# Kernel tuning notes

Measured on AMD Instinct MI355X. Metric: run time of the kernel, lower is better.

## Reference

```python
import jax, jax.numpy as jnp
import numpy as np

NB, DM, DIN, DS, DTR, K = 4, 64, 128, 16, 4, 4
C, COUT, H, W, BATCH, NH = 256, 256, 32, 32, 4, 8


def layernorm(x, w, b, eps=1e-5):
    mu = x.mean(-1, keepdims=True)
    var = ((x - mu) ** 2).mean(-1, keepdims=True)
    return (x - mu) * jax.lax.rsqrt(var + eps) * w + b


def ln_hw(x, eps=1e-5):
    # F.layer_norm(x, [H, W]) -> normalize over last two dims, no affine
    mu = x.mean((-2, -1), keepdims=True)
    var = ((x - mu) ** 2).mean((-2, -1), keepdims=True)
    return (x - mu) * jax.lax.rsqrt(var + eps)


def conv1d(x, w, b, groups=1, pad=1):
    # x: (B, Cin, L), w: (Cout, Cin//groups, k)
    y = jax.lax.conv_general_dilated(x, w, (1,), [(pad, pad)],
                                     dimension_numbers=('NCH', 'OIH', 'NCH'),
                                     feature_group_count=groups)
    return y + b[None, :, None]


def selective_scan(u, dt, Bm, Cm, A, Dp):
    # u, dt: (B,L,din); Bm, Cm: (B,L,ds); A: (din,ds); Dp: (din,)
    dA = jnp.exp(dt[..., None] * A)                     # (B,L,din,ds)
    dBu = (dt * u)[..., None] * Bm[:, :, None, :]       # (B,L,din,ds)

    def step(h, inp):
        dA_t, dBu_t, C_t = inp
        h = dA_t * h + dBu_t
        return h, jnp.einsum('bds,bs->bd', h, C_t)

    h0 = jnp.zeros((u.shape[0], DIN, DS), u.dtype)
    _, ys = jax.lax.scan(step, h0, (dA.transpose(1, 0, 2, 3), dBu.transpose(1, 0, 2, 3), Cm.transpose(1, 0, 2)))
    return ys.transpose(1, 0, 2) + u * Dp


def mamba(xs, inw, convw, convb, xpw, dtw, dtb, alog, dp, outw):
    # xs: (B,L,DM) one branch of Mamba(d_model=DM, d_state=DS, d_conv=K, expand=2)
    xz = xs @ inw.T                                     # (B,L,2*DIN)
    u, z = jnp.split(xz, 2, axis=-1)
    # causal depthwise conv1d (torch pads K-1 and truncates to L == left pad K-1)
    uc = jax.lax.conv_general_dilated(u.transpose(0, 2, 1), convw[:, None, :], (1,), [(K - 1, 0)],
                                      dimension_numbers=('NCH', 'OIH', 'NCH'),
                                      feature_group_count=DIN) + convb[None, :, None]
    u = jax.nn.silu(uc.transpose(0, 2, 1))              # (B,L,DIN)
    xdbc = u @ xpw.T                                    # (B,L,DTR+2*DS)
    dt = jax.nn.softplus(xdbc[..., :DTR] @ dtw.T + dtb)
    Bm, Cm = xdbc[..., DTR:DTR + DS], xdbc[..., DTR + DS:]
    y = selective_scan(u, dt, Bm, Cm, -jnp.exp(alog), dp)
    return (y * jax.nn.silu(z)) @ outw.T


mamba_v = jax.vmap(mamba)  # over branch axis 0 of inputs and all params


def mha(x, inw, inb, outw, outb):
    B, N, Cc = x.shape
    hd = Cc // NH
    qkv = x @ inw.T + inb
    q, k, v = jnp.split(qkv, 3, axis=-1)
    q = q.reshape(B, N, NH, hd).transpose(0, 2, 1, 3)
    k = k.reshape(B, N, NH, hd).transpose(0, 2, 1, 3)
    v = v.reshape(B, N, NH, hd).transpose(0, 2, 1, 3)
    att = jax.nn.softmax((q @ k.transpose(0, 1, 3, 2)) * (1.0 / (hd ** 0.5)), axis=-1)
    o = (att @ v).transpose(0, 2, 1, 3).reshape(B, N, Cc)
    return o @ outw.T + outb


def reference(x, norm_w, norm_b, skip_scale, m_inw, m_convw, m_convb, m_xpw, m_dtw, m_dtb, m_alog, m_d, m_outw, qdw_w, qdw_b, qpw_w, qpw_b, rdw_w, rdw_b, rpw_w, rpw_b, fdw_w, fdw_b, fpw_w, fpw_b, lc_w, lc_b, attn_inw, attn_inb, attn_outw, attn_outb, lgn_w, lgn_b, fc_w, fc_b, dwc_w, dwc_b, proj_w, proj_b):
    B, Cc, Hh, Ww = x.shape
    N = Hh * Ww
    xs = x.reshape(B, Cc, N).transpose(0, 2, 1)         # (B,N,C)
    xn = layernorm(xs, norm_w, norm_b)
    # channel-chunk into NB branches: (NB,B,N,DM)
    xc = xn.reshape(B, N, NB, DM).transpose(2, 0, 1, 3)
    xm = mamba_v(xc, m_inw, m_convw, m_convb, m_xpw, m_dtw, m_dtb, m_alog, m_d, m_outw) + skip_scale * xc
    x_concat = xm.transpose(1, 2, 0, 3).reshape(B, N, Cc)
    # branch gating: depthwise grouped conv (C->NB) then pointwise (NB->NB)
    Q = conv1d(conv1d(x_concat.transpose(0, 2, 1), qdw_w, qdw_b, groups=NB, pad=1), qpw_w, qpw_b, groups=1, pad=0)
    g = jax.nn.sigmoid(Q)                               # (B,NB,N)
    xg = (g.transpose(1, 0, 2)[..., None] * xm).transpose(1, 2, 0, 3).reshape(B, N, Cc)
    xgt = xg.transpose(0, 2, 1)                          # (B,C,N)
    R = conv1d(conv1d(xgt, rdw_w, rdw_b, groups=Cc, pad=1), rpw_w, rpw_b, groups=1, pad=0) + xgt
    cat = jnp.concatenate([xs, R.transpose(0, 2, 1)], axis=-1).transpose(0, 2, 1)  # (B,2C,N)
    xm2 = conv1d(conv1d(cat, fdw_w, fdw_b, groups=2 * Cc, pad=1), fpw_w, fpw_b, groups=1, pad=0) + cat[:, :Cc, :]
    xm2 = xm2.transpose(0, 2, 1)                         # (B,N,C)
    # local-global feature mixing
    x_local = conv1d(xm2.transpose(0, 2, 1), lc_w, lc_b, groups=Cc, pad=1).transpose(0, 2, 1)
    x_global = mha(xm2, attn_inw, attn_inb, attn_outw, attn_outb)
    x_out = jnp.concatenate([x_local, x_global], axis=-1) @ fc_w.T + fc_b
    x_out = jax.nn.gelu(layernorm(x_out, lgn_w, lgn_b), approximate=False)
    # DepthwiseConvolution: layer_norm over [H,W] (no affine) then depthwise conv2d
    xi = x_out.transpose(0, 2, 1).reshape(B, Cc, Hh, Ww)
    xi = ln_hw(xi)
    xi = jax.lax.conv_general_dilated(xi, dwc_w, (1, 1), [(1, 1), (1, 1)],
                                      dimension_numbers=('NCHW', 'OIHW', 'NCHW'),
                                      feature_group_count=Cc) + dwc_b[None, :, None, None]
    x_mixed = xi.reshape(B, Cc, N).transpose(0, 2, 1)
    x_mixed = layernorm(x_mixed, norm_w, norm_b)        # self.norm reused
    x_mixed = x_mixed @ proj_w.T + proj_b
    return x_mixed.transpose(0, 2, 1).reshape(B, COUT, Hh, Ww)


def setup_inputs() -> dict:
    key = jax.random.key(0)
    ks = iter(jax.random.split(key, 64))

    def rn(shape, s=0.02):
        return jax.random.normal(next(ks), shape, jnp.float32) * s

    return dict(
        x=jax.random.normal(next(ks), (BATCH, C, H, W), jnp.float32),
        norm_w=jnp.ones((C,), jnp.float32), norm_b=jnp.zeros((C,), jnp.float32),
        skip_scale=jnp.ones((1,), jnp.float32),
        m_inw=rn((NB, 2 * DIN, DM)), m_convw=rn((NB, DIN, K), 0.2), m_convb=jnp.zeros((NB, DIN), jnp.float32),
        m_xpw=rn((NB, DTR + 2 * DS, DIN)), m_dtw=rn((NB, DIN, DTR), 0.2), m_dtb=rn((NB, DIN), 0.5),
        m_alog=jnp.tile(jnp.log(jnp.arange(1, DS + 1, dtype=jnp.float32)), (NB, DIN, 1)),
        m_d=jnp.ones((NB, DIN), jnp.float32), m_outw=rn((NB, DM, DIN)),
        qdw_w=rn((NB, C // NB, 3), 0.1), qdw_b=jnp.zeros((NB,), jnp.float32),
        qpw_w=rn((NB, NB, 1), 0.3), qpw_b=jnp.zeros((NB,), jnp.float32),
        rdw_w=rn((C, 1, 3), 0.2), rdw_b=jnp.zeros((C,), jnp.float32),
        rpw_w=rn((C, C, 1)), rpw_b=jnp.zeros((C,), jnp.float32),
        fdw_w=rn((2 * C, 1, 3), 0.2), fdw_b=jnp.zeros((2 * C,), jnp.float32),
        fpw_w=rn((C, 2 * C, 1)), fpw_b=jnp.zeros((C,), jnp.float32),
        lc_w=rn((C, 1, 3), 0.2), lc_b=jnp.zeros((C,), jnp.float32),
        attn_inw=rn((3 * C, C)), attn_inb=jnp.zeros((3 * C,), jnp.float32),
        attn_outw=rn((C, C)), attn_outb=jnp.zeros((C,), jnp.float32),
        lgn_w=jnp.ones((C,), jnp.float32), lgn_b=jnp.zeros((C,), jnp.float32),
        fc_w=rn((C, 2 * C)), fc_b=jnp.zeros((C,), jnp.float32),
        dwc_w=rn((C, 1, 3, 3), 0.2), dwc_b=jnp.zeros((C,), jnp.float32),
        proj_w=rn((COUT, C)), proj_b=jnp.zeros((COUT,), jnp.float32),
    )
```

## Files before the change

kernel.cpp:

```cpp
#include <hip/hip_runtime.h>
#include <math.h>


namespace {
constexpr int NB_ = 4, DM_ = 64, DIN_ = 128, DS_ = 16, DTR_ = 4;
constexpr int C_ = 256, N_ = 1024, B_ = 4, HD_ = 32;
constexpr int NCH = 16, LCH = 64;
constexpr int NSTATE = 16 * 128 * 16;
}

typedef __attribute__((ext_vector_type(8))) short bf16x8;
typedef __attribute__((ext_vector_type(4))) float f32x4;
typedef __attribute__((ext_vector_type(8))) unsigned short ushort8v;
typedef __attribute__((ext_vector_type(4))) unsigned short ushort4v;

__device__ __forceinline__ unsigned short f2b(float f) {
  unsigned int u = __float_as_uint(f);
  unsigned int r = u + 0x7FFFu + ((u >> 16) & 1u);
  return (unsigned short)(r >> 16);
}
__device__ __forceinline__ float b2f(unsigned short u) {
  return __uint_as_float(((unsigned int)u) << 16);
}

__device__ __forceinline__ float2 blockReduce2(float a, float b, float* red) {
#pragma unroll
  for (int m = 1; m < 64; m <<= 1) {
    a += __shfl_xor(a, m, 64);
    b += __shfl_xor(b, m, 64);
  }
  int w = threadIdx.x >> 6;
  if ((threadIdx.x & 63) == 0) { red[2 * w] = a; red[2 * w + 1] = b; }
  __syncthreads();
  float ra = red[0] + red[2] + red[4] + red[6];
  float rb = red[1] + red[3] + red[5] + red[7];
  return make_float2(ra, rb);
}

__device__ __forceinline__ float siluf(float x) { return x / (1.f + expf(-x)); }
__device__ __forceinline__ float sigmf(float x) { return 1.f / (1.f + expf(-x)); }
__device__ __forceinline__ float softplusf(float x) {
  return fmaxf(x, 0.f) + log1pf(expf(-fabsf(x)));
}

__global__ __launch_bounds__(256) void k_ln_t2(const float* __restrict__ in,
                                               const float* __restrict__ w,
                                               const float* __restrict__ bias,
                                               unsigned short* __restrict__ out_ln) {
  __shared__ float tile[256][9];
  __shared__ float redp[32][8][2];
  __shared__ float stats[8][2];
  int bx = blockIdx.x;
  int b = bx >> 7, n0 = (bx & 127) * 8;
  int c = threadIdx.x;
  {
    const float* p = in + ((long)(b * C_ + c)) * N_ + n0;
#pragma unroll
    for (int j = 0; j < 8; ++j) tile[c][j] = p[j];
  }
  __syncthreads();
  {
    int n = c & 7, g = c >> 3;
    float a = 0.f, q = 0.f;
#pragma unroll
    for (int i = 0; i < 8; ++i) {
      float v = tile[g * 8 + i][n];
      a += v; q += v * v;
    }
    redp[g][n][0] = a; redp[g][n][1] = q;
  }
  __syncthreads();
  if (c < 8) {
    float a = 0.f, q = 0.f;
#pragma unroll
    for (int g2 = 0; g2 < 32; ++g2) { a += redp[g2][c][0]; q += redp[g2][c][1]; }
    float mu = a * (1.f / C_);
    float rs = rsqrtf(q * (1.f / C_) - mu * mu + 1e-5f);
    stats[c][0] = mu; stats[c][1] = rs;
  }
  __syncthreads();
  float wv = w[c], bv = bias[c];
#pragma unroll
  for (int j = 0; j < 8; ++j) {
    float v = tile[c][j];
    long o = ((long)(b * N_ + n0 + j)) * C_ + c;
    out_ln[o] = f2b((v - stats[j][0]) * stats[j][1] * wv + bv);
  }
}

__global__ __launch_bounds__(256) void k_inproj_conv(const unsigned short* __restrict__ xn,
                                                     const float* __restrict__ inw,
                                                     const float* __restrict__ cw,
                                                     const float* __restrict__ cb,
                                                     unsigned short* __restrict__ U,
                                                     unsigned short* __restrict__ Z) {
  __shared__ unsigned short xa[64][72];
  __shared__ unsigned short wb[64][72];
  __shared__ float ut[67][65];
  int r0 = blockIdx.x * 64;
  int nb = blockIdx.y >> 2, q = blockIdx.y & 3, c0 = q * 64;
  int t = threadIdx.x;
  int wv = t >> 6, lane = t & 63, g = lane >> 4, ql = lane & 15;
  const f32x4 zf = {0.f, 0.f, 0.f, 0.f};
  f32x4 acc[4] = {zf, zf, zf, zf};
  int rr = t >> 2, kq = (t & 3) * 16;
  {
    const unsigned short* xsrc = xn + (long)(r0 + rr) * C_ + nb * 64 + kq;
#pragma unroll
    for (int j = 0; j < 2; ++j)
      *(ushort8v*)&xa[rr][kq + 8 * j] = *(const ushort8v*)(xsrc + 8 * j);
    const float* wsrc = inw + ((long)nb * 256 + c0 + rr) * 64 + kq;
#pragma unroll
    for (int j = 0; j < 4; ++j) {
      float4 v = *(const float4*)(wsrc + 4 * j);
      ushort4v u = {f2b(v.x), f2b(v.y), f2b(v.z), f2b(v.w)};
      *(ushort4v*)&wb[rr][kq + 4 * j] = u;
    }
  }
  __syncthreads();
#pragma unroll
  for (int ks = 0; ks < 2; ++ks) {
    bf16x8 a = *(const bf16x8*)&xa[wv * 16 + ql][ks * 32 + g * 8];
#pragma unroll
    for (int ct = 0; ct < 4; ++ct) {
      bf16x8 b = *(const bf16x8*)&wb[ct * 16 + ql][ks * 32 + g * 8];
      acc[ct] = __builtin_amdgcn_mfma_f32_16x16x32_bf16(a, b, acc[ct], 0, 0, 0);
    }
  }
  if (q < 2) {
#pragma unroll
    for (int ct = 0; ct < 4; ++ct)
#pragma unroll
      for (int reg = 0; reg < 4; ++reg)
        ut[3 + wv * 16 + g * 4 + reg][ct * 16 + ql] = acc[ct][reg];
    if (t < 192) {
      int hr = t >> 6, lc = t & 63;
      float hv = 0.f;
      if ((r0 & 1023) != 0) {
        const unsigned short* xrow = xn + (long)(r0 - 3 + hr) * C_ + nb * 64;
        const float* wrow = inw + ((long)nb * 256 + c0 + lc) * 64;
#pragma unroll 8
        for (int k = 0; k < 64; ++k) hv += b2f(xrow[k]) * wrow[k];
      }
      ut[hr][lc] = hv;
    }
    __syncthreads();
#pragma unroll
    for (int ct = 0; ct < 4; ++ct) {
      int lc = ct * 16 + ql;
      int d = c0 + lc;
      const float* cwp = cw + (nb * DIN_ + d) * 4;
      float w0 = cwp[0], w1 = cwp[1], w2 = cwp[2], w3 = cwp[3];
      float bv = cb[nb * DIN_ + d];
#pragma unroll
      for (int reg = 0; reg < 4; ++reg) {
        int lr = wv * 16 + g * 4 + reg;
        float a = bv + w3 * ut[3 + lr][lc] + w2 * ut[2 + lr][lc] +
                  w1 * ut[1 + lr][lc] + w0 * ut[lr][lc];
        long row = (long)nb * 4096 + r0 + lr;
        U[row * DIN_ + d] = f2b(siluf(a));
      }
    }
  } else {
#pragma unroll
    for (int ct = 0; ct < 4; ++ct) {
      int col = c0 - 128 + ct * 16 + ql;
#pragma unroll
      for (int reg = 0; reg < 4; ++reg) {
        long row = (long)nb * 4096 + r0 + wv * 16 + g * 4 + reg;
        Z[row * DIN_ + col] = f2b(acc[ct][reg]);
      }
    }
  }
}

__global__ __launch_bounds__(256) void k_xdbc_scanA(const unsigned short* __restrict__ U,
                                                    const float* __restrict__ xpw,
                                                    const float* __restrict__ dtw,
                                                    const float* __restrict__ dtb,
                                                    const float* __restrict__ alog,
                                                    float* __restrict__ DT,
                                                    float* __restrict__ BMb,
                                                    float* __restrict__ CMb,
                                                    float* __restrict__ Aprod,
                                                    float* __restrict__ Hend) {
  __shared__ unsigned short u_sb[64][136];
  __shared__ unsigned short wb[48][72];
  __shared__ float xd_s[64][40];
  __shared__ float dtw_s[128][4];
  __shared__ float dtb_s[128];
  __shared__ float dt_s[64][132];
  __shared__ float bm_s[64][20];
  int t = threadIdx.x;
  long row0 = (long)blockIdx.x * 64;
  int nb = blockIdx.x >> 6;
  int nbb = blockIdx.x >> 4, chunk = blockIdx.x & 15;
  for (int i = t; i < 512; i += 256) dtw_s[i >> 2][i & 3] = dtw[nb * 512 + i];
  if (t < 128) dtb_s[t] = dtb[nb * DIN_ + t];
  int wv = t >> 6, lane = t & 63, g = lane >> 4, ql = lane & 15;
  const f32x4 zf = {0.f, 0.f, 0.f, 0.f};
  f32x4 acc[3] = {zf, zf, zf};
  int rr = t >> 2, kq = (t & 3) * 16;
  for (int k0 = 0; k0 < 128; k0 += 64) {
    __syncthreads();
    const unsigned short* xsrc = U + (row0 + rr) * DIN_ + k0 + kq;
#pragma unroll
    for (int j = 0; j < 2; ++j)
      *(ushort8v*)&u_sb[rr][k0 + kq + 8 * j] = *(const ushort8v*)(xsrc + 8 * j);
    if (rr < 48) {
      if (rr < 36) {
        const float* wsrc = xpw + (long)nb * 36 * 128 + rr * 128 + k0 + kq;
#pragma unroll
        for (int j = 0; j < 4; ++j) {
          float4 v = *(const float4*)(wsrc + 4 * j);
          ushort4v u = {f2b(v.x), f2b(v.y), f2b(v.z), f2b(v.w)};
          *(ushort4v*)&wb[rr][kq + 4 * j] = u;
        }
      } else {
        ushort4v z = {0, 0, 0, 0};
#pragma unroll
        for (int j = 0; j < 4; ++j) *(ushort4v*)&wb[rr][kq + 4 * j] = z;
      }
    }
    __syncthreads();
#pragma unroll
    for (int ks = 0; ks < 2; ++ks) {
      bf16x8 a = *(const bf16x8*)&u_sb[wv * 16 + ql][k0 + ks * 32 + g * 8];
#pragma unroll
      for (int ct = 0; ct < 3; ++ct) {
        bf16x8 b = *(const bf16x8*)&wb[ct * 16 + ql][ks * 32 + g * 8];
        acc[ct] = __builtin_amdgcn_mfma_f32_16x16x32_bf16(a, b, acc[ct], 0, 0, 0);
      }
    }
  }
#pragma unroll
  for (int ct = 0; ct < 3; ++ct) {
    int col = ct * 16 + ql;
    if (col < 36) {
#pragma unroll
      for (int reg = 0; reg < 4; ++reg)
        xd_s[wv * 16 + g * 4 + reg][col] = acc[ct][reg];
    }
  }
  __syncthreads();
  {
    int r = t >> 2, sq = (t & 3) * 4;
    float4 bm4 = make_float4(xd_s[r][4 + sq], xd_s[r][5 + sq],
                             xd_s[r][6 + sq], xd_s[r][7 + sq]);
    *(float4*)&BMb[(row0 + r) * DS_ + sq] = bm4;
    *(float4*)&bm_s[r][sq] = bm4;
    float4 cm4 = make_float4(xd_s[r][20 + sq], xd_s[r][21 + sq],
                             xd_s[r][22 + sq], xd_s[r][23 + sq]);
    *(float4*)&CMb[(row0 + r) * DS_ + sq] = cm4;
  }
  {
    int r = t >> 2, dg = t & 3;
    float x0 = xd_s[r][0], x1 = xd_s[r][1], x2 = xd_s[r][2], x3 = xd_s[r][3];
    float* dst = DT + (row0 + r) * DIN_ + dg * 32;
#pragma unroll
    for (int j = 0; j < 8; ++j) {
      float o[4];
#pragma unroll
      for (int e = 0; e < 4; ++e) {
        int d = dg * 32 + j * 4 + e;
        float a = dtb_s[d] + x0 * dtw_s[d][0] + x1 * dtw_s[d][1] +
                  x2 * dtw_s[d][2] + x3 * dtw_s[d][3];
        o[e] = softplusf(a);
      }
      float4 o4 = make_float4(o[0], o[1], o[2], o[3]);
      *(float4*)(dst + j * 4) = o4;
      *(float4*)&dt_s[r][dg * 32 + j * 4] = o4;
    }
  }
  __syncthreads();
  {
    int dl = t >> 2, sg = t & 3;
#pragma unroll
    for (int dh = 0; dh < 2; ++dh) {
      int d = dh * 64 + dl;
      float A[4];
#pragma unroll
      for (int i = 0; i < 4; ++i)
        A[i] = -expf(alog[(nb * DIN_ + d) * DS_ + sg * 4 + i]);
      float h[4] = {0.f, 0.f, 0.f, 0.f};
      float ap[4] = {1.f, 1.f, 1.f, 1.f};
      for (int tt = 0; tt < LCH; ++tt) {
        float dtv = dt_s[tt][d];
        float uv  = b2f(u_sb[tt][d]);
        float cc = dtv * uv;
        float4 bm4 = *(const float4*)&bm_s[tt][sg * 4];
        float bmv[4] = {bm4.x, bm4.y, bm4.z, bm4.w};
#pragma unroll
        for (int i = 0; i < 4; ++i) {
          float dA = __expf(dtv * A[i]);
          h[i] = dA * h[i] + cc * bmv[i];
          ap[i] *= dA;
        }
      }
      long st = (long)chunk * NSTATE + ((nbb << 7) + d) * 16 + sg * 4;
      *(float4*)&Aprod[st] = make_float4(ap[0], ap[1], ap[2], ap[3]);
      *(float4*)&Hend[st]  = make_float4(h[0], h[1], h[2], h[3]);
    }
  }
}

__global__ __launch_bounds__(256) void k_scanC(float* __restrict__ DT,
                                               const unsigned short* __restrict__ U,
                                               const float* __restrict__ BMb,
                                               const float* __restrict__ CMb,
                                               const float* __restrict__ alog,
                                               const float* __restrict__ Dp,
                                               const float* __restrict__ Aprod,
                                               const float* __restrict__ Hend) {
  __shared__ float dt_s[64][64];
  __shared__ float u_s[64][64];
  __shared__ float bm_s[64][16];
  __shared__ float cm_s[64][16];
  int bx = blockIdx.x;
  int chunk = bx >> 5, rem = bx & 31, nbb = rem >> 1, dh = rem & 1;
  int nb = nbb >> 2;
  int t = threadIdx.x;
  int dl = t >> 2, sg = t & 3;
  int d = dh * 64 + dl;
  long base = (long)nbb * N_ + chunk * LCH;
#pragma unroll
  for (int j = 0; j < 4; ++j) {
    int f = t + 256 * j;
    int tt = f >> 4, dq = (f & 15) * 4;
    long src = (base + tt) * DIN_ + dh * 64 + dq;
    *(float4*)&dt_s[tt][dq] = *(const float4*)&DT[src];
    ushort4v u4 = *(const ushort4v*)&U[src];
    u_s[tt][dq + 0] = b2f(u4[0]);
    u_s[tt][dq + 1] = b2f(u4[1]);
    u_s[tt][dq + 2] = b2f(u4[2]);
    u_s[tt][dq + 3] = b2f(u4[3]);
  }
  {
    int tt = t >> 2, sq = (t & 3) * 4;
    *(float4*)&bm_s[tt][sq] = *(const float4*)&BMb[(base + tt) * DS_ + sq];
    *(float4*)&cm_s[tt][sq] = *(const float4*)&CMb[(base + tt) * DS_ + sq];
  }
  float A[4];
#pragma unroll
  for (int i = 0; i < 4; ++i)
    A[i] = -expf(alog[(nb * DIN_ + d) * DS_ + sg * 4 + i]);
  float Dv = Dp[nb * DIN_ + d];
  float h[4] = {0.f, 0.f, 0.f, 0.f};
  {
    long state4 = ((nbb << 7) + d) * 16 + sg * 4;
    for (int c = 0; c < chunk; ++c) {
      float4 a4 = *(const float4*)&Aprod[(long)c * NSTATE + state4];
      float4 e4 = *(const float4*)&Hend[(long)c * NSTATE + state4];
      h[0] = e4.x + a4.x * h[0];
      h[1] = e4.y + a4.y * h[1];
      h[2] = e4.z + a4.z * h[2];
      h[3] = e4.w + a4.w * h[3];
    }
  }
  __syncthreads();
  for (int tt = 0; tt < LCH; ++tt) {
    float dtv = dt_s[tt][dl];
    float uv  = u_s[tt][dl];
    float cc = dtv * uv;
    float4 bm4 = *(const float4*)&bm_s[tt][sg * 4];
    float4 cm4 = *(const float4*)&cm_s[tt][sg * 4];
    float bmv[4] = {bm4.x, bm4.y, bm4.z, bm4.w};
    float cmv[4] = {cm4.x, cm4.y, cm4.z, cm4.w};
    float p = 0.f;
#pragma unroll
    for (int i = 0; i < 4; ++i) {
      float dA = __expf(dtv * A[i]);
      h[i] = dA * h[i] + cc * bmv[i];
      p += h[i] * cmv[i];
    }
    p += __shfl_xor(p, 1, 64);
    p += __shfl_xor(p, 2, 64);
    if (sg == 0) DT[(base + tt) * DIN_ + d] = p + Dv * uv;
  }
}

__global__ __launch_bounds__(256) void k_outproj_mfma(const float* __restrict__ Y,
                                                      const unsigned short* __restrict__ Zb,
                                                      const float* __restrict__ outw,
                                                      const unsigned short* __restrict__ xn,
                                                      const float* __restrict__ skip,
                                                      float* __restrict__ XMC) {
  __shared__ unsigned short xa[32][72];
  __shared__ unsigned short wb[64][72];
  int r0 = blockIdx.x * 32;
  int nb = blockIdx.y;
  int t = threadIdx.x;
  int w = t >> 6, lane = t & 63, g = lane >> 4, ql = lane & 15;
  int rg = w & 1, cp = w >> 1;
  const f32x4 zf = {0.f, 0.f, 0.f, 0.f};
  f32x4 acc[2] = {zf, zf};
  int ar = t >> 3, ak = (t & 7) * 8;
  int wr = t >> 2, wk = (t & 3) * 16;
  for (int k0 = 0; k0 < 128; k0 += 64) {
    __syncthreads();
    long row = (long)nb * 4096 + r0 + ar;
    const float* ysrc = Y + row * DIN_ + k0 + ak;
    const unsigned short* zsrc = Zb + row * DIN_ + k0 + ak;
#pragma unroll
    for (int j = 0; j < 2; ++j) {
      float4 yv = *(const float4*)(ysrc + 4 * j);
      ushort4v z4 = *(const ushort4v*)(zsrc + 4 * j);
      ushort4v u = {f2b(yv.x * siluf(b2f(z4[0]))), f2b(yv.y * siluf(b2f(z4[1]))),
                    f2b(yv.z * siluf(b2f(z4[2]))), f2b(yv.w * siluf(b2f(z4[3])))};
      *(ushort4v*)&xa[ar][ak + 4 * j] = u;
    }
    const float* wsrc = outw + ((long)nb * 64 + wr) * 128 + k0 + wk;
#pragma unroll
    for (int j = 0; j < 4; ++j) {
      float4 v = *(const float4*)(wsrc + 4 * j);
      ushort4v u = {f2b(v.x), f2b(v.y), f2b(v.z), f2b(v.w)};
      *(ushort4v*)&wb[wr][wk + 4 * j] = u;
    }
    __syncthreads();
#pragma unroll
    for (int ks = 0; ks < 2; ++ks) {
      bf16x8 a = *(const bf16x8*)&xa[rg * 16 + ql][ks * 32 + g * 8];
#pragma unroll
      for (int ct = 0; ct < 2; ++ct) {
        bf16x8 b = *(const bf16x8*)&wb[(cp * 2 + ct) * 16 + ql][ks * 32 + g * 8];
        acc[ct] = __builtin_amdgcn_mfma_f32_16x16x32_bf16(a, b, acc[ct], 0, 0, 0);
      }
    }
  }
  float sk = skip[0];
#pragma unroll
  for (int ct = 0; ct < 2; ++ct) {
    int col = (cp * 2 + ct) * 16 + ql;
#pragma unroll
    for (int reg = 0; reg < 4; ++reg) {
      int bn = r0 + rg * 16 + g * 4 + reg;
      long oc = (long)bn * C_ + nb * 64 + col;
      XMC[oc] = acc[ct][reg] + sk * b2f(xn[oc]);
    }
  }
}

__global__ __launch_bounds__(128) void k_gate(const float* __restrict__ XMC,
                                              const float* __restrict__ qdw_w,
                                              const float* __restrict__ qdw_b,
                                              const float* __restrict__ qpw_w,
                                              const float* __restrict__ qpw_b,
                                              float* __restrict__ G) {
  int t = threadIdx.x;
  int gid = (blockIdx.x * 128 + t) >> 4;
  int cq = t & 3, p = (t >> 2) & 3;
  int b = gid >> 10, n = gid & 1023;
  float a = 0.f;
#pragma unroll
  for (int k = 0; k < 3; ++k) {
    int nn = n + k - 1;
    if (nn < 0 || nn >= N_) continue;
    const float* xr = XMC + ((long)b * N_ + nn) * C_ + p * 64 + cq * 16;
    const float* wr = qdw_w + (p * 64 + cq * 16) * 3 + k;
    float xv[16];
    *(float4*)&xv[0]  = *(const float4*)(xr);
    *(float4*)&xv[4]  = *(const float4*)(xr + 4);
    *(float4*)&xv[8]  = *(const float4*)(xr + 8);
    *(float4*)&xv[12] = *(const float4*)(xr + 12);
#pragma unroll
    for (int i = 0; i < 16; ++i) a += xv[i] * wr[i * 3];
  }
  a += __shfl_xor(a, 1, 64);
  a += __shfl_xor(a, 2, 64);
  float q1 = a + qdw_b[p];
  int lane = t & 63;
  float q1g[4];
#pragma unroll
  for (int pp = 0; pp < 4; ++pp) q1g[pp] = __shfl(q1, (lane & ~12) | (pp << 2), 64);
  int o = p;
  float r = qpw_b[o];
#pragma unroll
  for (int pp = 0; pp < 4; ++pp) r += qpw_w[o * 4 + pp] * q1g[pp];
  if (cq == 0) G[((long)b * 4 + o) * N_ + n] = sigmf(r);
}

__global__ __launch_bounds__(256) void k_xg(const float* __restrict__ XMC,
                                            const float* __restrict__ G,
                                            float* __restrict__ XG) {
  __shared__ float tile[64][33];
  int bx = blockIdx.x;
  int b = bx >> 7, ct = (bx >> 5) & 3, nt = bx & 31;
  int c0 = ct * 64, n0 = nt * 32;
  int t = threadIdx.x;
  {
    int cc = t & 63, nq = t >> 6;
#pragma unroll
    for (int j = 0; j < 8; ++j) {
      int nn = nq * 8 + j;
      tile[cc][nn] = XMC[((long)(b * N_ + n0 + nn)) * C_ + c0 + cc];
    }
  }
  __syncthreads();
  {
    int nl = t & 31, cq = t >> 5;
    float g = G[((long)(b * 4 + ct)) * N_ + n0 + nl];
#pragma unroll
    for (int j = 0; j < 8; ++j) {
      int cl = cq * 8 + j;
      XG[((long)(b * C_ + c0 + cl)) * N_ + n0 + nl] = g * tile[cl][nl];
    }
  }
}

template <int KD>
__global__ __launch_bounds__(256) void k_gemm_cm_dw(const float* __restrict__ inA,
                                                    const float* __restrict__ inB,
                                                    const float* __restrict__ dww,
                                                    const float* __restrict__ dwb,
                                                    const float* __restrict__ w,
                                                    const float* __restrict__ bias,
                                                    const float* __restrict__ residCM,
                                                    const float* __restrict__ residXCM,
                                                    float* __restrict__ outCM,
                                                    unsigned short* __restrict__ outRMb) {
  __shared__ unsigned short xa[32][72];
  __shared__ unsigned short wb[64][72];
  int rb = blockIdx.x;
  int b = rb >> 5, n0 = (rb & 31) * 32;
  int c0 = blockIdx.y * 64;
  int t = threadIdx.x;
  int w8 = t >> 6, lane = t & 63, g = lane >> 4, ql = lane & 15;
  int rg = w8 & 1, cp = w8 >> 1;
  const f32x4 zf = {0.f, 0.f, 0.f, 0.f};
  f32x4 acc[2] = {zf, zf};
  int cr = t >> 2, nq = (t & 3) * 8;
  int wr = t >> 2, wk = (t & 3) * 16;
  for (int k0 = 0; k0 < KD; k0 += 64) {
    __syncthreads();
    {
      int k = k0 + cr;
      const float* src = (inB != nullptr && k >= 256)
                             ? inB + ((long)(b * 256 + k - 256)) * 1024
                             : inA + ((long)(b * 256 + k)) * 1024;
      float w0 = dww[k * 3], w1 = dww[k * 3 + 1], w2 = dww[k * 3 + 2], bv = dwb[k];
#pragma unroll
      for (int j = 0; j < 2; ++j) {
        int nb4 = n0 + nq + 4 * j;
        float4 v = *(const float4*)&src[nb4];
        float vm1 = (nb4 > 0) ? src[nb4 - 1] : 0.f;
        float vp4 = (nb4 + 4 < 1024) ? src[nb4 + 4] : 0.f;
        xa[nq + 4 * j + 0][cr] = f2b(bv + w0 * vm1 + w1 * v.x + w2 * v.y);
        xa[nq + 4 * j + 1][cr] = f2b(bv + w0 * v.x + w1 * v.y + w2 * v.z);
        xa[nq + 4 * j + 2][cr] = f2b(bv + w0 * v.y + w1 * v.z + w2 * v.w);
        xa[nq + 4 * j + 3][cr] = f2b(bv + w0 * v.z + w1 * v.w + w2 * vp4);
      }
    }
    const float* wsrc = w + (long)(c0 + wr) * KD + k0 + wk;
#pragma unroll
    for (int j = 0; j < 4; ++j) {
      float4 v = *(const float4*)(wsrc + 4 * j);
      ushort4v u = {f2b(v.x), f2b(v.y), f2b(v.z), f2b(v.w)};
      *(ushort4v*)&wb[wr][wk + 4 * j] = u;
    }
    __syncthreads();
#pragma unroll
    for (int ks = 0; ks < 2; ++ks) {
      bf16x8 a = *(const bf16x8*)&xa[rg * 16 + ql][ks * 32 + g * 8];
#pragma unroll
      for (int ct = 0; ct < 2; ++ct) {
        bf16x8 bfr = *(const bf16x8*)&wb[(cp * 2 + ct) * 16 + ql][ks * 32 + g * 8];
        acc[ct] = __builtin_amdgcn_mfma_f32_16x16x32_bf16(a, bfr, acc[ct], 0, 0, 0);
      }
    }
  }
#pragma unroll
  for (int ct = 0; ct < 2; ++ct) {
    int col = c0 + (cp * 2 + ct) * 16 + ql;
    float bv = bias[col];
    if (outCM) {
      long base = ((long)(b * 256 + col)) * 1024 + n0 + rg * 16 + g * 4;
      float4 r4 = *(const float4*)(residCM + base);
      float4 o = make_float4(acc[ct][0] + bv + r4.x, acc[ct][1] + bv + r4.y,
                             acc[ct][2] + bv + r4.z, acc[ct][3] + bv + r4.w);
      *(float4*)(outCM + base) = o;
    } else {
      int nbase = n0 + rg * 16 + g * 4;
      float4 r4 = *(const float4*)&residXCM[((long)(b * 256 + col)) * 1024 + nbase];
      float rv[4] = {r4.x, r4.y, r4.z, r4.w};
#pragma unroll
      for (int reg = 0; reg < 4; ++reg) {
        long row = (long)b * 1024 + nbase + reg;
        outRMb[row * 256 + col] = f2b(acc[ct][reg] + bv + rv[reg]);
      }
    }
  }
}

__global__ __launch_bounds__(256) void k_gemm_qkv(const unsigned short* __restrict__ in,
                                                  const float* __restrict__ w,
                                                  const float* __restrict__ bias,
                                                  unsigned short* __restrict__ out) {
  __shared__ unsigned short xa[64][72];
  __shared__ unsigned short wb[64][72];
  int r0 = blockIdx.x * 64;
  int c0 = blockIdx.y * 64;
  int t = threadIdx.x;
  int wv = t >> 6, lane = t & 63, g = lane >> 4, ql = lane & 15;
  const f32x4 zf = {0.f, 0.f, 0.f, 0.f};
  f32x4 acc[4] = {zf, zf, zf, zf};
  int rr = t >> 2, kq = (t & 3) * 16;
  for (int k0 = 0; k0 < 256; k0 += 64) {
    __syncthreads();
    const unsigned short* xsrc = in + (long)(r0 + rr) * 256 + k0 + kq;
#pragma unroll
    for (int j = 0; j < 2; ++j)
      *(ushort8v*)&xa[rr][kq + 8 * j] = *(const ushort8v*)(xsrc + 8 * j);
    const float* wsrc = w + (long)(c0 + rr) * 256 + k0 + kq;
#pragma unroll
    for (int j = 0; j < 4; ++j) {
      float4 v = *(const float4*)(wsrc + 4 * j);
      ushort4v u = {f2b(v.x), f2b(v.y), f2b(v.z), f2b(v.w)};
      *(ushort4v*)&wb[rr][kq + 4 * j] = u;
    }
    __syncthreads();
#pragma unroll
    for (int ks = 0; ks < 2; ++ks) {
      bf16x8 a = *(const bf16x8*)&xa[wv * 16 + ql][ks * 32 + g * 8];
#pragma unroll
      for (int ct = 0; ct < 4; ++ct) {
        bf16x8 b = *(const bf16x8*)&wb[ct * 16 + ql][ks * 32 + g * 8];
        acc[ct] = __builtin_amdgcn_mfma_f32_16x16x32_bf16(a, b, acc[ct], 0, 0, 0);
      }
    }
  }
#pragma unroll
  for (int ct = 0; ct < 4; ++ct) {
    int col = c0 + ct * 16 + ql;
    float bv = bias[col];
#pragma unroll
    for (int reg = 0; reg < 4; ++reg) {
      long row = r0 + wv * 16 + g * 4 + reg;
      out[row * 768 + col] = f2b(acc[ct][reg] + bv);
    }
  }
}

__global__ __launch_bounds__(256) void k_gemm_attnout(const unsigned short* __restrict__ inA,
                                                      const float* __restrict__ w,
                                                      const float* __restrict__ bias,
                                                      unsigned short* __restrict__ out) {
  __shared__ unsigned short xa[32][72];
  __shared__ unsigned short wb[64][72];
  int r0 = blockIdx.x * 32;
  int c0 = blockIdx.y * 64;
  int t = threadIdx.x;
  int w8 = t >> 6, lane = t & 63, g = lane >> 4, ql = lane & 15;
  int rg = w8 & 1, cp = w8 >> 1;
  const f32x4 zf = {0.f, 0.f, 0.f, 0.f};
  f32x4 acc[2] = {zf, zf};
  int ar = t >> 3, ak = (t & 7) * 8;
  int wr = t >> 2, wk = (t & 3) * 16;
  for (int k0 = 0; k0 < 256; k0 += 64) {
    __syncthreads();
    const unsigned short* xsrc = inA + (long)(r0 + ar) * 256 + k0 + ak;
    *(ushort8v*)&xa[ar][ak] = *(const ushort8v*)xsrc;
    const float* wsrc = w + (long)(c0 + wr) * 256 + k0 + wk;
#pragma unroll
    for (int j = 0; j < 4; ++j) {
      float4 v = *(const float4*)(wsrc + 4 * j);
      ushort4v u = {f2b(v.x), f2b(v.y), f2b(v.z), f2b(v.w)};
      *(ushort4v*)&wb[wr][wk + 4 * j] = u;
    }
    __syncthreads();
#pragma unroll
    for (int ks = 0; ks < 2; ++ks) {
      bf16x8 a = *(const bf16x8*)&xa[rg * 16 + ql][ks * 32 + g * 8];
#pragma unroll
      for (int ct = 0; ct < 2; ++ct) {
        bf16x8 b = *(const bf16x8*)&wb[(cp * 2 + ct) * 16 + ql][ks * 32 + g * 8];
        acc[ct] = __builtin_amdgcn_mfma_f32_16x16x32_bf16(a, b, acc[ct], 0, 0, 0);
      }
    }
  }
#pragma unroll
  for (int ct = 0; ct < 2; ++ct) {
    int col = c0 + (cp * 2 + ct) * 16 + ql;
    float bv = bias[col];
#pragma unroll
    for (int reg = 0; reg < 4; ++reg) {
      long row = r0 + rg * 16 + g * 4 + reg;
      out[row * 256 + col] = f2b(acc[ct][reg] + bv);
    }
  }
}

__global__ __launch_bounds__(256) void k_gemm_fc(const unsigned short* __restrict__ XM2,
                                                 const unsigned short* __restrict__ XGL,
                                                 const float* __restrict__ lcw,
                                                 const float* __restrict__ lcb,
                                                 const float* __restrict__ w,
                                                 const float* __restrict__ bias,
                                                 unsigned short* __restrict__ out) {
  __shared__ unsigned short xa[32][72];
  __shared__ unsigned short wb[64][72];
  int r0 = blockIdx.x * 32;
  int c0 = blockIdx.y * 64;
  int t = threadIdx.x;
  int w8 = t >> 6, lane = t & 63, g = lane >> 4, ql = lane & 15;
  int rg = w8 & 1, cp = w8 >> 1;
  const f32x4 zf = {0.f, 0.f, 0.f, 0.f};
  f32x4 acc[2] = {zf, zf};
  int ar = t >> 3, ak = (t & 7) * 8;
  int wr = t >> 2, wk = (t & 3) * 16;
  for (int k0 = 0; k0 < 512; k0 += 64) {
    __syncthreads();
    int kk = k0 + ak;
    long row = r0 + ar;
    if (kk < 256) {
      int n = (int)(row & 1023);
      const unsigned short* pc = XM2 + row * 256 + kk;
      bool hm = n > 0, hp = n < 1023;
#pragma unroll
      for (int j = 0; j < 2; ++j) {
        ushort4v v4 = *(const ushort4v*)(pc + 4 * j);
        ushort4v zm = {0, 0, 0, 0};
        ushort4v vm4 = hm ? *(const ushort4v*)(pc - 256 + 4 * j) : zm;
        ushort4v vp4 = hp ? *(const ushort4v*)(pc + 256 + 4 * j) : zm;
        int c = kk + 4 * j;
#pragma unroll
        for (int e = 0; e < 4; ++e) {
          float vv = b2f(v4[e]);
          float vmv = hm ? b2f(vm4[e]) : 0.f;
          float vpv = hp ? b2f(vp4[e]) : 0.f;
          xa[ar][ak + 4 * j + e] = f2b(lcb[c + e] + lcw[(c + e) * 3] * vmv +
                                       lcw[(c + e) * 3 + 1] * vv +
                                       lcw[(c + e) * 3 + 2] * vpv);
        }
      }
    } else {
      const unsigned short* xsrc = XGL + row * 256 + (kk - 256);
      *(ushort8v*)&xa[ar][ak] = *(const ushort8v*)xsrc;
    }
    const float* wsrc = w + (long)(c0 + wr) * 512 + k0 + wk;
#pragma unroll
    for (int j = 0; j < 4; ++j) {
      float4 v = *(const float4*)(wsrc + 4 * j);
      ushort4v u = {f2b(v.x), f2b(v.y), f2b(v.z), f2b(v.w)};
      *(ushort4v*)&wb[wr][wk + 4 * j] = u;
    }
    __syncthreads();
#pragma unroll
    for (int ks = 0; ks < 2; ++ks) {
      bf16x8 a = *(const bf16x8*)&xa[rg * 16 + ql][ks * 32 + g * 8];
#pragma unroll
      for (int ct = 0; ct < 2; ++ct) {
        bf16x8 b = *(const bf16x8*)&wb[(cp * 2 + ct) * 16 + ql][ks * 32 + g * 8];
        acc[ct] = __builtin_amdgcn_mfma_f32_16x16x32_bf16(a, b, acc[ct], 0, 0, 0);
      }
    }
  }
#pragma unroll
  for (int ct = 0; ct < 2; ++ct) {
    int col = c0 + (cp * 2 + ct) * 16 + ql;
    float bv = bias[col];
#pragma unroll
    for (int reg = 0; reg < 4; ++reg) {
      long row = r0 + rg * 16 + g * 4 + reg;
      out[row * 256 + col] = f2b(acc[ct][reg] + bv);
    }
  }
}

__global__ __launch_bounds__(256) void k_attn_mfma(const unsigned short* __restrict__ qkvb,
                                                   unsigned short* __restrict__ Ob) {
  __shared__ unsigned short K_lds[64 * 40];
  __shared__ unsigned short Vt_lds[32 * 72];
  __shared__ unsigned short P_lds[4][16 * 72];
  int bx = blockIdx.x;
  int bh = bx >> 4, qt = bx & 15;
  int b = bh >> 3, h = bh & 7;
  int t = threadIdx.x;
  int w = t >> 6, lane = t & 63;
  int g = lane >> 4, ql = lane & 15;
  const float qscale = 0.17677669529663687f * 1.44269504088896341f;

  bf16x8 q_frag = *(const bf16x8*)(qkvb + ((long)(b * N_ + qt * 64 + w * 16 + ql)) * 768 + h * HD_ + g * 8);
  float m = -1e30f, l = 0.f;
  f32x4 o_acc[2];
  const f32x4 zf = {0.f, 0.f, 0.f, 0.f};
  o_acc[0] = zf; o_acc[1] = zf;

  for (int kt = 0; kt < 16; ++kt) {
    __syncthreads();
    {
      int kr = t >> 2, d0 = (t & 3) * 8;
      const unsigned short* gp = qkvb + ((long)(b * N_ + kt * 64 + kr)) * 768 + 256 + h * HD_ + d0;
      ushort8v kv = *(const ushort8v*)gp;
      *(ushort8v*)&K_lds[kr * 40 + d0] = kv;
      ushort8v vv = *(const ushort8v*)(gp + 256);
#pragma unroll
      for (int i = 0; i < 8; ++i) Vt_lds[(d0 + i) * 72 + kr] = vv[i];
    }
    __syncthreads();
    f32x4 s_frag[4];
#pragma unroll
    for (int s = 0; s < 4; ++s) {
      bf16x8 k_frag = *(const bf16x8*)&K_lds[(s * 16 + ql) * 40 + g * 8];
      s_frag[s] = __builtin_amdgcn_mfma_f32_16x16x32_bf16(k_frag, q_frag, zf, 0, 0, 0);
    }
    float sv[16];
#pragma unroll
    for (int s = 0; s < 4; ++s)
#pragma unroll
      for (int r = 0; r < 4; ++r) sv[s * 4 + r] = s_frag[s][r] * qscale;
    float tmax = sv[0];
#pragma unroll
    for (int i = 1; i < 16; ++i) tmax = fmaxf(tmax, sv[i]);
    tmax = fmaxf(tmax, __shfl_xor(tmax, 16));
    tmax = fmaxf(tmax, __shfl_xor(tmax, 32));
    float mn = fmaxf(m, tmax);
    float corr = exp2f(m - mn);
    float psum = 0.f;
    unsigned short pb[16];
#pragma unroll
    for (int i = 0; i < 16; ++i) {
      float p = exp2f(sv[i] - mn);
      psum += p;
      pb[i] = f2b(p);
    }
    psum += __shfl_xor(psum, 16);
    psum += __shfl_xor(psum, 32);
    l = l * corr + psum;
    m = mn;
#pragma unroll
    for (int mt = 0; mt < 2; ++mt)
#pragma unroll
      for (int r = 0; r < 4; ++r) o_acc[mt][r] *= corr;
#pragma unroll
    for (int s = 0; s < 4; ++s) {
      ushort4v p4 = {pb[s * 4], pb[s * 4 + 1], pb[s * 4 + 2], pb[s * 4 + 3]};
      *(ushort4v*)&P_lds[w][ql * 72 + s * 16 + g * 4] = p4;
    }
#pragma unroll
    for (int c = 0; c < 2; ++c) {
      bf16x8 p_frag = *(const bf16x8*)&P_lds[w][ql * 72 + c * 32 + g * 8];
#pragma unroll
      for (int mt = 0; mt < 2; ++mt) {
        bf16x8 v_frag = *(const bf16x8*)&Vt_lds[(mt * 16 + ql) * 72 + c * 32 + g * 8];
        o_acc[mt] = __builtin_amdgcn_mfma_f32_16x16x32_bf16(v_frag, p_frag, o_acc[mt], 0, 0, 0);
      }
    }
  }
  float inv = 1.f / l;
  unsigned short* op = Ob + ((long)(b * N_ + qt * 64 + w * 16 + ql)) * C_ + h * HD_;
#pragma unroll
  for (int mt = 0; mt < 2; ++mt) {
    ushort4v o4 = {f2b(o_acc[mt][0] * inv), f2b(o_acc[mt][1] * inv),
                   f2b(o_acc[mt][2] * inv), f2b(o_acc[mt][3] * inv)};
    *(ushort4v*)(op + mt * 16 + g * 4) = o4;
  }
}

__global__ __launch_bounds__(256) void k_lngelu(const unsigned short* __restrict__ XO,
                                                const float* __restrict__ lw,
                                                const float* __restrict__ lb,
                                                unsigned short* __restrict__ XI) {
  __shared__ float tile[256][9];
  __shared__ float redp[32][8][2];
  __shared__ float stats[8][2];
  int bx = blockIdx.x;
  int b = bx >> 7, n0 = (bx & 127) * 8;
  int c = threadIdx.x;
#pragma unroll
  for (int j = 0; j < 8; ++j)
    tile[c][j] = b2f(XO[((long)(b * N_ + n0 + j)) * C_ + c]);
  __syncthreads();
  {
    int n = c & 7, g = c >> 3;
    float a = 0.f, q = 0.f;
#pragma unroll
    for (int i = 0; i < 8; ++i) {
      float v = tile[g * 8 + i][n];
      a += v; q += v * v;
    }
    redp[g][n][0] = a; redp[g][n][1] = q;
  }
  __syncthreads();
  if (c < 8) {
    float a = 0.f, q = 0.f;
#pragma unroll
    for (int g2 = 0; g2 < 32; ++g2) { a += redp[g2][c][0]; q += redp[g2][c][1]; }
    float mu = a * (1.f / C_);
    float rs = rsqrtf(q * (1.f / C_) - mu * mu + 1e-5f);
    stats[c][0] = mu; stats[c][1] = rs;
  }
  __syncthreads();
  float wv = lw[c], bv = lb[c];
  float o[8];
#pragma unroll
  for (int j = 0; j < 8; ++j) {
    float x = (tile[c][j] - stats[j][0]) * stats[j][1] * wv + bv;
    o[j] = 0.5f * x * (1.f + erff(x * 0.70710678118654752f));
  }
  unsigned short* dst = &XI[((long)(b * C_ + c)) * N_ + n0];
#pragma unroll
  for (int j4 = 0; j4 < 2; ++j4) {
    ushort4v o4 = {f2b(o[4 * j4]), f2b(o[4 * j4 + 1]), f2b(o[4 * j4 + 2]), f2b(o[4 * j4 + 3])};
    *(ushort4v*)(dst + j4 * 4) = o4;
  }
}

__global__ __launch_bounds__(256) void k_lnhw_dwc(const unsigned short* __restrict__ XIin,
                                                  const float* __restrict__ w,
                                                  const float* __restrict__ bias,
                                                  unsigned short* __restrict__ XD) {
  __shared__ float pl[32][33];
  __shared__ float red[8];
  long base = (long)blockIdx.x * 1024;
  int c = blockIdx.x & 255;
  int t = threadIdx.x;
  ushort4v v4 = *(const ushort4v*)&XIin[base + t * 4];
  float vx = b2f(v4[0]), vy = b2f(v4[1]), vz = b2f(v4[2]), vw = b2f(v4[3]);
  float a = vx + vy + vz + vw;
  float q = vx * vx + vy * vy + vz * vz + vw * vw;
  float2 s = blockReduce2(a, q, red);
  float mu = s.x * (1.f / 1024.f);
  float rs = rsqrtf(s.y * (1.f / 1024.f) - mu * mu + 1e-5f);
  int hh = t >> 3, w0 = (t & 7) * 4;
  pl[hh][w0 + 0] = (vx - mu) * rs;
  pl[hh][w0 + 1] = (vy - mu) * rs;
  pl[hh][w0 + 2] = (vz - mu) * rs;
  pl[hh][w0 + 3] = (vw - mu) * rs;
  __syncthreads();
  float wk[9];
#pragma unroll
  for (int i = 0; i < 9; ++i) wk[i] = w[c * 9 + i];
  float bv = bias[c];
  float o[4];
#pragma unroll
  for (int j = 0; j < 4; ++j) {
    int ww = w0 + j;
    float acc = bv;
#pragma unroll
    for (int kh = 0; kh < 3; ++kh) {
      int h2 = hh + kh - 1;
      if (h2 < 0 || h2 >= 32) continue;
#pragma unroll
      for (int kw = 0; kw < 3; ++kw) {
        int w2 = ww + kw - 1;
        if (w2 < 0 || w2 >= 32) continue;
        acc += wk[kh * 3 + kw] * pl[h2][w2];
      }
    }
    o[j] = acc;
  }
  ushort4v o4 = {f2b(o[0]), f2b(o[1]), f2b(o[2]), f2b(o[3])};
  *(ushort4v*)&XD[base + t * 4] = o4;
}

__global__ __launch_bounds__(256) void k_lnproj(const unsigned short* __restrict__ XD,
                                                const float* __restrict__ nw,
                                                const float* __restrict__ nbias,
                                                const float* __restrict__ w,
                                                const float* __restrict__ bias,
                                                float* __restrict__ out) {
  __shared__ unsigned short xa[32][72];
  __shared__ unsigned short wb[64][72];
  __shared__ float ps[8][32], pq[8][32];
  __shared__ float mu_s[32], rs_s[32];
  int rb = blockIdx.x;
  int b = rb >> 5, n0 = (rb & 31) * 32;
  int c0 = blockIdx.y * 64;
  int t = threadIdx.x;
  {
    int nl = t & 31, cq = t >> 5;
    const unsigned short* src = XD + ((long)(b * 256 + cq * 32)) * 1024 + n0 + nl;
    float s = 0.f, q = 0.f;
    for (int i = 0; i < 32; ++i) {
      float v = b2f(src[(long)i * 1024]);
      s += v; q += v * v;
    }
    ps[cq][nl] = s; pq[cq][nl] = q;
  }
  __syncthreads();
  if (t < 32) {
    float s = 0.f, q = 0.f;
#pragma unroll
    for (int g2 = 0; g2 < 8; ++g2) { s += ps[g2][t]; q += pq[g2][t]; }
    float mu = s * (1.f / 256.f);
    float rs = rsqrtf(q * (1.f / 256.f) - mu * mu + 1e-5f);
    mu_s[t] = mu; rs_s[t] = rs;
  }
  int w8 = t >> 6, lane = t & 63, g = lane >> 4, ql = lane & 15;
  int rg = w8 & 1, cp = w8 >> 1;
  const f32x4 zf = {0.f, 0.f, 0.f, 0.f};
  f32x4 acc[2] = {zf, zf};
  int rr = t >> 2, nq = (t & 3) * 8;
  int wr = t >> 2, wk = (t & 3) * 16;
  for (int k0 = 0; k0 < 256; k0 += 64) {
    __syncthreads();
    {
      int ch = k0 + rr;
      const unsigned short* src = XD + ((long)(b * 256 + ch)) * 1024 + n0 + nq;
      float wv_ = nw[ch], bv_ = nbias[ch];
      ushort8v v8 = *(const ushort8v*)src;
#pragma unroll
      for (int e = 0; e < 8; ++e) {
        int n = nq + e;
        xa[n][rr] = f2b((b2f(v8[e]) - mu_s[n]) * rs_s[n] * wv_ + bv_);
      }
      const float* wsrc = w + (long)(c0 + wr) * 256 + k0 + wk;
#pragma unroll
      for (int j = 0; j < 4; ++j) {
        float4 v = *(const float4*)(wsrc + 4 * j);
        ushort4v u = {f2b(v.x), f2b(v.y), f2b(v.z), f2b(v.w)};
        *(ushort4v*)&wb[wr][wk + 4 * j] = u;
      }
    }
    __syncthreads();
#pragma unroll
    for (int ks = 0; ks < 2; ++ks) {
      bf16x8 a = *(const bf16x8*)&xa[rg * 16 + ql][ks * 32 + g * 8];
#pragma unroll
      for (int ct = 0; ct < 2; ++ct) {
        bf16x8 bfr = *(const bf16x8*)&wb[(cp * 2 + ct) * 16 + ql][ks * 32 + g * 8];
        acc[ct] = __builtin_amdgcn_mfma_f32_16x16x32_bf16(a, bfr, acc[ct], 0, 0, 0);
      }
    }
  }
#pragma unroll
  for (int ct = 0; ct < 2; ++ct) {
    int col = c0 + (cp * 2 + ct) * 16 + ql;
    float bv = bias[col];
    long basei = ((long)(b * 256 + col)) * 1024 + n0 + rg * 16 + g * 4;
    *(float4*)(out + basei) = make_float4(acc[ct][0] + bv, acc[ct][1] + bv,
                                          acc[ct][2] + bv, acc[ct][3] + bv);
  }
}

extern "C" void kernel_launch(void* const* d_in, const int* in_sizes, int n_in,
                              void* d_out, int out_size, void* d_ws, size_t ws_size,
                              hipStream_t stream) {
  const float* x        = (const float*)d_in[0];
  const float* norm_w   = (const float*)d_in[1];
  const float* norm_b   = (const float*)d_in[2];
  const float* skip     = (const float*)d_in[3];
  const float* m_inw    = (const float*)d_in[4];
  const float* m_convw  = (const float*)d_in[5];
  const float* m_convb  = (const float*)d_in[6];
  const float* m_xpw    = (const float*)d_in[7];
  const float* m_dtw    = (const float*)d_in[8];
  const float* m_dtb    = (const float*)d_in[9];
  const float* m_alog   = (const float*)d_in[10];
  const float* m_d      = (const float*)d_in[11];
  const float* m_outw   = (const float*)d_in[12];
  const float* qdw_w    = (const float*)d_in[13];
  const float* qdw_b    = (const float*)d_in[14];
  const float* qpw_w    = (const float*)d_in[15];
  const float* qpw_b    = (const float*)d_in[16];
  const float* rdw_w    = (const float*)d_in[17];
  const float* rdw_b    = (const float*)d_in[18];
  const float* rpw_w    = (const float*)d_in[19];
  const float* rpw_b    = (const float*)d_in[20];
  const float* fdw_w    = (const float*)d_in[21];
  const float* fdw_b    = (const float*)d_in[22];
  const float* fpw_w    = (const float*)d_in[23];
  const float* fpw_b    = (const float*)d_in[24];
  const float* lc_w     = (const float*)d_in[25];
  const float* lc_b     = (const float*)d_in[26];
  const float* attn_inw = (const float*)d_in[27];
  const float* attn_inb = (const float*)d_in[28];
  const float* attn_outw= (const float*)d_in[29];
  const float* attn_outb= (const float*)d_in[30];
  const float* lgn_w    = (const float*)d_in[31];
  const float* lgn_b    = (const float*)d_in[32];
  const float* fc_w     = (const float*)d_in[33];
  const float* fc_b     = (const float*)d_in[34];
  const float* dwc_w    = (const float*)d_in[35];
  const float* dwc_b    = (const float*)d_in[36];
  const float* proj_w   = (const float*)d_in[37];
  const float* proj_b   = (const float*)d_in[38];
  float* out = (float*)d_out;

  float* ws = (float*)d_ws;
  const size_t F = 1048576;
  unsigned short* XNB = (unsigned short*)(ws + 1 * F);
  unsigned short* UB  = (unsigned short*)(ws + 2 * F);
  unsigned short* ZB  = (unsigned short*)(ws + 4 * F);
  float* DT  = ws + 6 * F;
  float* BM  = ws + 8 * F;
  float* CM  = ws + 8 * F + F / 4;
  float* XMC = ws + 8 * F + F / 2;
  float* SC_APROD = ws + 8 * F + F / 2;
  float* SC_HEND  = ws + 9 * F;
  float* G   = ws + 0 * F;
  float* XG  = ws + 2 * F;
  float* RB  = ws + 4 * F + F / 2;
  unsigned short* XM2B = (unsigned short*)(ws + 5 * F + F / 2);
  unsigned short* QKVB = (unsigned short*)(ws + 1 * F);
  unsigned short* OB   = (unsigned short*)(ws + 4 * F);
  unsigned short* XGLB = (unsigned short*)(ws + 6 * F);
  unsigned short* XOB  = (unsigned short*)(ws + 7 * F);
  unsigned short* XIB  = (unsigned short*)(ws + 8 * F);
  unsigned short* XDB  = (unsigned short*)(ws + 0 * F);
  (void)ws_size; (void)in_sizes; (void)n_in; (void)out_size;

  k_ln_t2<<<512, 256, 0, stream>>>(x, norm_w, norm_b, XNB);
  k_inproj_conv<<<dim3(64, 16), 256, 0, stream>>>(XNB, m_inw, m_convw, m_convb, UB, ZB);
  k_xdbc_scanA<<<256, 256, 0, stream>>>(UB, m_xpw, m_dtw, m_dtb, m_alog,
                                        DT, BM, CM, SC_APROD, SC_HEND);
  k_scanC<<<512, 256, 0, stream>>>(DT, UB, BM, CM, m_alog, m_d, SC_APROD, SC_HEND);
  k_outproj_mfma<<<dim3(128, 4), 256, 0, stream>>>(DT, ZB, m_outw, XNB, skip, XMC);
  k_gate<<<512, 128, 0, stream>>>(XMC, qdw_w, qdw_b, qpw_w, qpw_b, G);
  k_xg<<<512, 256, 0, stream>>>(XMC, G, XG);
  k_gemm_cm_dw<256><<<dim3(128, 4), 256, 0, stream>>>(XG, nullptr, rdw_w, rdw_b,
                                                      rpw_w, rpw_b, XG, nullptr, RB, nullptr);
  k_gemm_cm_dw<512><<<dim3(128, 4), 256, 0, stream>>>(x, RB, fdw_w, fdw_b,
                                                      fpw_w, fpw_b, nullptr, x, nullptr, XM2B);
  k_gemm_qkv<<<dim3(64, 12), 256, 0, stream>>>(XM2B, attn_inw, attn_inb, QKVB);
  k_attn_mfma<<<512, 256, 0, stream>>>(QKVB, OB);
  k_gemm_attnout<<<dim3(128, 4), 256, 0, stream>>>(OB, attn_outw, attn_outb, XGLB);
  k_gemm_fc<<<dim3(128, 4), 256, 0, stream>>>(XM2B, XGLB, lc_w, lc_b, fc_w, fc_b, XOB);
  k_lngelu<<<512, 256, 0, stream>>>(XOB, lgn_w, lgn_b, XIB);
  k_lnhw_dwc<<<1024, 256, 0, stream>>>(XIB, dwc_w, dwc_b, XDB);
  k_lnproj<<<dim3(128, 4), 256, 0, stream>>>(XDB, norm_w, norm_b, proj_w, proj_b, out);
}
```

Measured before the change: 185.5 us.

## Fuse gate computation and gated transpose into one kernel via shared tile

Merges the gate kernel (depthwise conv plus pointwise mix plus sigmoid) with the gated transpose kernel. Each block loads a 256x18 halo tile of XMC into shared memory once, computes the 16x4 gate values from it, and writes the transposed, gated output with float4 stores. This removes one launch, the intermediate G buffer round trip and the duplicate reads of XMC. In exchange the grid shrinks to 256 blocks and the tile loads are strided per thread.

```diff
diff --git a/kernel.cpp b/kernel.cpp
--- a/kernel.cpp
+++ b/kernel.cpp
@@ -440,69 +440,64 @@
   }
 }
 
-__global__ __launch_bounds__(128) void k_gate(const float* __restrict__ XMC,
-                                              const float* __restrict__ qdw_w,
-                                              const float* __restrict__ qdw_b,
-                                              const float* __restrict__ qpw_w,
-                                              const float* __restrict__ qpw_b,
-                                              float* __restrict__ G) {
+__global__ __launch_bounds__(256) void k_gatexg(const float* __restrict__ XMC,
+                                                const float* __restrict__ qdw_w,
+                                                const float* __restrict__ qdw_b,
+                                                const float* __restrict__ qpw_w,
+                                                const float* __restrict__ qpw_b,
+                                                float* __restrict__ XG) {
+  __shared__ float tile[256][19];
+  __shared__ float gg[16][4];
+  int bx = blockIdx.x;
+  int b = bx >> 6, nt = bx & 63, n0 = nt * 16;
   int t = threadIdx.x;
-  int gid = (blockIdx.x * 128 + t) >> 4;
-  int cq = t & 3, p = (t >> 2) & 3;
-  int b = gid >> 10, n = gid & 1023;
-  float a = 0.f;
-#pragma unroll
-  for (int k = 0; k < 3; ++k) {
-    int nn = n + k - 1;
-    if (nn < 0 || nn >= N_) continue;
-    const float* xr = XMC + ((long)b * N_ + nn) * C_ + p * 64 + cq * 16;
-    const float* wr = qdw_w + (p * 64 + cq * 16) * 3 + k;
-    float xv[16];
-    *(float4*)&xv[0]  = *(const float4*)(xr);
-    *(float4*)&xv[4]  = *(const float4*)(xr + 4);
-    *(float4*)&xv[8]  = *(const float4*)(xr + 8);
-    *(float4*)&xv[12] = *(const float4*)(xr + 12);
-#pragma unroll
-    for (int i = 0; i < 16; ++i) a += xv[i] * wr[i * 3];
-  }
-  a += __shfl_xor(a, 1, 64);
-  a += __shfl_xor(a, 2, 64);
-  float q1 = a + qdw_b[p];
-  int lane = t & 63;
-  float q1g[4];
-#pragma unroll
-  for (int pp = 0; pp < 4; ++pp) q1g[pp] = __shfl(q1, (lane & ~12) | (pp << 2), 64);
-  int o = p;
-  float r = qpw_b[o];
-#pragma unroll
-  for (int pp = 0; pp < 4; ++pp) r += qpw_w[o * 4 + pp] * q1g[pp];
-  if (cq == 0) G[((long)b * 4 + o) * N_ + n] = sigmf(r);
-}
-
-__global__ __launch_bounds__(256) void k_xg(const float* __restrict__ XMC,
-                                            const float* __restrict__ G,
-                                            float* __restrict__ XG) {
-  __shared__ float tile[64][33];
-  int bx = blockIdx.x;
-  int b = bx >> 7, ct = (bx >> 5) & 3, nt = bx & 31;
-  int c0 = ct * 64, n0 = nt * 32;
-  int t = threadIdx.x;
-  {
-    int cc = t & 63, nq = t >> 6;
-#pragma unroll
-    for (int j = 0; j < 8; ++j) {
-      int nn = nq * 8 + j;
-      tile[cc][nn] = XMC[((long)(b * N_ + n0 + nn)) * C_ + c0 + cc];
-    }
-  }
-  __syncthreads();
-  {
-    int nl = t & 31, cq = t >> 5;
-    float g = G[((long)(b * 4 + ct)) * N_ + n0 + nl];
-#pragma unroll
-    for (int j = 0; j < 8; ++j) {
-      int cl = cq * 8 + j;
-      XG[((long)(b * C_ + c0 + cl)) * N_ + n0 + nl] = g * tile[cl][nl];
+  {
+    int c = t;
+#pragma unroll 6
+    for (int j = 0; j < 18; ++j) {
+      int nn = n0 - 1 + j;
+      tile[c][j] = (nn >= 0 && nn < N_) ? XMC[((long)(b * N_ + nn)) * C_ + c] : 0.f;
+    }
+  }
+  __syncthreads();
+  {
+    int n = t >> 4, p = (t >> 2) & 3, cq = t & 3;
+    float a = 0.f;
+#pragma unroll
+    for (int k = 0; k < 3; ++k) {
+      int nn = n0 + n + k - 1;
+      if (nn < 0 || nn >= N_) continue;
+      int j = n + k;
+      const float* wr = qdw_w + (p * 64 + cq * 16) * 3 + k;
+      int cbase = p * 64 + cq * 16;
+#pragma unroll
+      for (int i = 0; i < 16; ++i) a += tile[cbase + i][j] * wr[i * 3];
+    }
+    a += __shfl_xor(a, 1, 64);
+    a += __shfl_xor(a, 2, 64);
+    float q1 = a + qdw_b[p];
+    int lane = t & 63;
+    float q1g[4];
+#pragma unroll
+    for (int pp = 0; pp < 4; ++pp) q1g[pp] = __shfl(q1, (lane & ~15) | (pp << 2), 64);
+    float r = qpw_b[p];
+#pragma unroll
+    for (int pp = 0; pp < 4; ++pp) r += qpw_w[p * 4 + pp] * q1g[pp];
+    if (cq == 0) gg[n][p] = sigmf(r);
+  }
+  __syncthreads();
+  {
+    int cb = t >> 2, nq = (t & 3) * 4;
+#pragma unroll
+    for (int rep = 0; rep < 4; ++rep) {
+      int c = cb + rep * 64;
+      int p = c >> 6;
+      float4 o;
+      o.x = gg[nq + 0][p] * tile[c][1 + nq + 0];
+      o.y = gg[nq + 1][p] * tile[c][1 + nq + 1];
+      o.z = gg[nq + 2][p] * tile[c][1 + nq + 2];
+      o.w = gg[nq + 3][p] * tile[c][1 + nq + 3];
+      *(float4*)&XG[((long)(b * C_ + c)) * N_ + n0 + nq] = o;
     }
   }
 }
@@ -1088,7 +1083,6 @@
   float* XMC = ws + 8 * F + F / 2;
   float* SC_APROD = ws + 8 * F + F / 2;
   float* SC_HEND  = ws + 9 * F;
-  float* G   = ws + 0 * F;
   float* XG  = ws + 2 * F;
   float* RB  = ws + 4 * F + F / 2;
   unsigned short* XM2B = (unsigned short*)(ws + 5 * F + F / 2);
@@ -1106,8 +1100,7 @@
                                         DT, BM, CM, SC_APROD, SC_HEND);
   k_scanC<<<512, 256, 0, stream>>>(DT, UB, BM, CM, m_alog, m_d, SC_APROD, SC_HEND);
   k_outproj_mfma<<<dim3(128, 4), 256, 0, stream>>>(DT, ZB, m_outw, XNB, skip, XMC);
-  k_gate<<<512, 128, 0, stream>>>(XMC, qdw_w, qdw_b, qpw_w, qpw_b, G);
-  k_xg<<<512, 256, 0, stream>>>(XMC, G, XG);
+  k_gatexg<<<256, 256, 0, stream>>>(XMC, qdw_w, qdw_b, qpw_w, qpw_b, XG);
   k_gemm_cm_dw<256><<<dim3(128, 4), 256, 0, stream>>>(XG, nullptr, rdw_w, rdw_b,
                                                       rpw_w, rpw_b, XG, nullptr, RB, nullptr);
   k_gemm_cm_dw<512><<<dim3(128, 4), 256, 0, stream>>>(x, RB, fdw_w, fdw_b,
```

New measurement: 184.6 us. No clear change (-0.5%).
